# Kernel optimization log

Measured on AMD Instinct MI355X. Metric: run time of the kernel, lower is better.

The kernel has to match this reference:

```python
import jax, jax.numpy as jnp
import numpy as np
from functools import partial

TOP_K = 2
LN_EPS = 1e-5


def setup_inputs() -> dict:
    key = jax.random.key(0)
    ks = jax.random.split(key, 4)
    B, T, H, F, E = 2, 2048, 1024, 4096, 8
    hidden_states = jax.random.normal(ks[0], (B, T, H), dtype=jnp.float32)
    # Router weights: original inits to zeros; use small random so routing is non-degenerate.
    router_w = jax.random.normal(ks[1], (E, H), dtype=jnp.float32) * 0.02
    router_b = jnp.zeros((E,), dtype=jnp.float32)
    W1 = jax.random.normal(ks[2], (E, H, F), dtype=jnp.float32) * (1.0 / np.sqrt(H))
    b1 = jnp.zeros((E, F), dtype=jnp.float32)
    W2 = jax.random.normal(ks[3], (E, F, H), dtype=jnp.float32) * (1.0 / np.sqrt(F))
    b2 = jnp.zeros((E, H), dtype=jnp.float32)
    ln_gamma = jnp.ones((H,), dtype=jnp.float32)
    ln_beta = jnp.zeros((H,), dtype=jnp.float32)
    return {"hidden_states": hidden_states, "router_w": router_w, "router_b": router_b,
            "W1": W1, "b1": b1, "W2": W2, "b2": b2,
            "ln_gamma": ln_gamma, "ln_beta": ln_beta}


def _layer_norm(x, gamma, beta):
    mu = jnp.mean(x, axis=-1, keepdims=True)
    var = jnp.var(x, axis=-1, keepdims=True)
    return (x - mu) * jax.lax.rsqrt(var + LN_EPS) * gamma + beta


def _moe_forward(hidden_states, router_w, router_b, W1, b1, W2, b2, ln_gamma, ln_beta):
    B, T, H = hidden_states.shape
    E = router_w.shape[0]
    N = B * T
    x = hidden_states.reshape(N, H)
    # Router (jitter=0.0, eval mode): logits [N, E]
    logits = x @ router_w.T + router_b
    topk_vals, topk_idx = jax.lax.top_k(logits, TOP_K)        # [N, K]
    topk_w = jax.nn.softmax(topk_vals, axis=-1)               # [N, K]
    # Scatter top-k weights into a dense combine matrix [N, E] (zeros elsewhere).
    probs = jnp.zeros((N, E), dtype=x.dtype).at[jnp.arange(N)[:, None], topk_idx].set(topk_w)
    # Per-expert FFN via scan over the (small, fixed) expert axis; each step is one
    # big GEMM over all tokens weighted by that expert's combine prob (0 for
    # tokens not routed to it) — same math as gather/MLP/scatter with no capacity drop.
    def body(acc, params_e):
        Wa, ba, Wb, bb, pe = params_e          # pe: [N]
        h = jax.nn.gelu(x @ Wa + ba, approximate=False)   # [N, F]
        y = h @ Wb + bb                                    # [N, H]
        return acc + y * pe[:, None], None
    out, _ = jax.lax.scan(body, jnp.zeros_like(x), (W1, b1, W2, b2, probs.T))
    out = out.reshape(B, T, H)
    return _layer_norm(out + hidden_states, ln_gamma, ln_beta)


def reference(hidden_states, router_w, router_b, W1, b1, W2, b2, ln_gamma, ln_beta):
    return _moe_forward(hidden_states, router_w, router_b, W1, b1, W2, b2, ln_gamma, ln_beta)
```

## Files before the change

### kernel.cpp

```cpp
#include <hip/hip_runtime.h>
#include <hip/hip_bf16.h>


typedef unsigned short u16;
typedef unsigned int u32;
typedef __attribute__((ext_vector_type(4))) float f32x4;
typedef __attribute__((ext_vector_type(8))) short s16x8;
typedef __attribute__((ext_vector_type(8))) unsigned short u16x8;

#define GLD16(gp, lp) __builtin_amdgcn_global_load_lds( \
    (const __attribute__((address_space(1))) void*)(gp), \
    (__attribute__((address_space(3))) void*)(lp), 16, 0, 0)

__device__ __forceinline__ u16 f2bf(float f) {
    union { float f; u32 u; } v; v.f = f;
    u32 u = v.u;
    return (u16)((u + 0x7fffu + ((u >> 16) & 1u)) >> 16);
}

__device__ __forceinline__ float gelu_f(float v) {
    const float u = v * (0.7978845608f + 0.0356774081f * v * v);
    const float t = __expf(-2.0f * u);
    return v * __builtin_amdgcn_rcpf(1.0f + t);
}

__global__ void k_init(int* cc) { if (threadIdx.x < 16) cc[threadIdx.x] = 0; }

__global__ __launch_bounds__(256) void k_router(
    const float* __restrict__ x, const float* __restrict__ rw, const float* __restrict__ rb,
    u16* __restrict__ xb, int* __restrict__ eidx, float* __restrict__ wgt, int* __restrict__ counts)
{
    const int wav = threadIdx.x >> 6, lane = threadIdx.x & 63;
    const int t = blockIdx.x * 4 + wav;
    const float* xt = x + (size_t)t * 1024;
    float acc[8] = {0.f,0.f,0.f,0.f,0.f,0.f,0.f,0.f};
    #pragma unroll
    for (int c = 0; c < 4; c++) {
        const int base = c * 256 + lane * 4;
        const float4 xv = *(const float4*)(xt + base);
        ushort4 pk;
        pk.x = f2bf(xv.x); pk.y = f2bf(xv.y); pk.z = f2bf(xv.z); pk.w = f2bf(xv.w);
        *(ushort4*)(xb + (size_t)t * 1024 + base) = pk;
        #pragma unroll
        for (int e = 0; e < 8; e++) {
            const float4 wv = *(const float4*)(rw + e * 1024 + base);
            acc[e] += xv.x * wv.x + xv.y * wv.y + xv.z * wv.z + xv.w * wv.w;
        }
    }
    #pragma unroll
    for (int e = 0; e < 8; e++) {
        #pragma unroll
        for (int s = 32; s; s >>= 1) acc[e] += __shfl_xor(acc[e], s);
    }
    if (lane == 0) {
        float v0 = -3e38f, v1 = -3e38f; int i0 = 0, i1 = 0;
        #pragma unroll
        for (int e = 0; e < 8; e++) {
            const float l = acc[e] + rb[e];
            if (l > v0) { v1 = v0; i1 = i0; v0 = l; i0 = e; }
            else if (l > v1) { v1 = l; i1 = e; }
        }
        const float w0 = 1.0f / (1.0f + expf(v1 - v0));
        eidx[2 * t] = i0; eidx[2 * t + 1] = i1;
        wgt[2 * t] = w0; wgt[2 * t + 1] = 1.0f - w0;
        atomicAdd(&counts[i0], 1); atomicAdd(&counts[i1], 1);
    }
}

__global__ void k_offsets(const int* __restrict__ counts, int* __restrict__ offsets) {
    if (threadIdx.x == 0) {
        int s = 0;
        for (int e = 0; e < 8; e++) { offsets[e] = s; s += counts[e]; }
        offsets[8] = s;
    }
}

__global__ __launch_bounds__(256) void k_place(
    const int* __restrict__ eidx, const int* __restrict__ offsets, int* __restrict__ cursors,
    int* __restrict__ rows, int* __restrict__ pos_of)
{
    const int a = blockIdx.x * 256 + threadIdx.x;
    const int e = eidx[a];
    const int pos = offsets[e] + atomicAdd(&cursors[e], 1);
    rows[pos] = a >> 1;
    pos_of[a] = pos;
}

__global__ __launch_bounds__(256) void k_transp(
    const float* __restrict__ src, u16* __restrict__ dst, int R, int C)
{
    const int e = blockIdx.z;
    const float* s = src + (size_t)e * R * C;
    u16* d = dst + (size_t)e * R * C;
    const int c = blockIdx.x * 64 + (threadIdx.x >> 2);
    const int r0 = blockIdx.y * 32 + (threadIdx.x & 3) * 8;
    u16x8 v;
    #pragma unroll
    for (int k = 0; k < 8; k++)
        v[k] = f2bf(s[(size_t)(r0 + k) * C + c]);
    *(u16x8*)(d + (size_t)c * R + r0) = v;
}

__global__ __launch_bounds__(256) void k_gemm1(
    const u16* __restrict__ xb, const u16* __restrict__ W1t, const float* __restrict__ b1,
    u16* __restrict__ hbuf, const int* __restrict__ rows, const int* __restrict__ offsets)
{
    const int e = blockIdx.z;
    const int off = offsets[e], cnt = offsets[e + 1] - off;
    const int row0 = blockIdx.y * 128;
    if (row0 >= cnt) return;
    const int n0 = blockIdx.x * 128;
    const int tid = threadIdx.x;
    const int lane = tid & 63, wav = tid >> 6;

    __shared__ u16 At[128][32];
    __shared__ u16 Bt[128][32];

    const int ar0 = tid >> 2, ar1 = ar0 + 64;
    const int cl8 = (tid & 3) * 8;
    const int t0 = rows[off + min(row0 + ar0, cnt - 1)];
    const int t1 = rows[off + min(row0 + ar1, cnt - 1)];
    const u16* a_src0 = xb + (size_t)t0 * 1024 + cl8;
    const u16* a_src1 = xb + (size_t)t1 * 1024 + cl8;
    const u16* b_src0 = W1t + ((size_t)e * 4096 + n0 + ar0) * 1024 + cl8;
    const u16* b_src1 = W1t + ((size_t)e * 4096 + n0 + ar1) * 1024 + cl8;

    char* a_d0 = (char*)At + wav * 1024;
    char* a_d1 = (char*)At + 4096 + wav * 1024;
    char* b_d0 = (char*)Bt + wav * 1024;
    char* b_d1 = (char*)Bt + 4096 + wav * 1024;

    f32x4 acc[4][4] = {};
    const int wr = wav >> 1, wc = wav & 1;
    const int koff = (lane >> 4) * 8;
    const u16* Ab = &At[wr * 64 + (lane & 15)][koff];
    const u16* Bb = &Bt[wc * 64 + (lane & 15)][koff];

    for (int k0 = 0; k0 < 1024; k0 += 32) {
        GLD16(a_src0 + k0, a_d0);
        GLD16(a_src1 + k0, a_d1);
        GLD16(b_src0 + k0, b_d0);
        GLD16(b_src1 + k0, b_d1);
        __syncthreads();
        s16x8 af[4], bfr[4];
        #pragma unroll
        for (int i = 0; i < 4; i++) {
            af[i]  = *(const s16x8*)(Ab + i * 512);
            bfr[i] = *(const s16x8*)(Bb + i * 512);
        }
        #pragma unroll
        for (int mi = 0; mi < 4; mi++)
            #pragma unroll
            for (int ni = 0; ni < 4; ni++)
                acc[mi][ni] = __builtin_amdgcn_mfma_f32_16x16x32_bf16(af[mi], bfr[ni], acc[mi][ni], 0, 0, 0);
        __syncthreads();
    }

    const int rb4 = (lane >> 4) * 4;
    #pragma unroll
    for (int mi = 0; mi < 4; mi++) {
        #pragma unroll
        for (int j = 0; j < 4; j++) {
            const int lrow = wr * 64 + mi * 16 + rb4 + j;
            if (row0 + lrow < cnt) {
                const size_t gr = (size_t)(off + row0 + lrow);
                #pragma unroll
                for (int ni = 0; ni < 4; ni++) {
                    const int col = n0 + wc * 64 + ni * 16 + (lane & 15);
                    const float v = acc[mi][ni][j] + b1[e * 4096 + col];
                    hbuf[gr * 4096 + col] = f2bf(gelu_f(v));
                }
            }
        }
    }
}

__global__ __launch_bounds__(256) void k_gemm2(
    const u16* __restrict__ hbuf, const u16* __restrict__ W2t, const float* __restrict__ b2,
    float* __restrict__ y0, float* __restrict__ y1, const int* __restrict__ offsets)
{
    const int e = blockIdx.z >> 1, kh = blockIdx.z & 1;
    const int off = offsets[e], cnt = offsets[e + 1] - off;
    const int row0 = blockIdx.y * 128;
    if (row0 >= cnt) return;
    const int n0 = blockIdx.x * 128;
    const int tid = threadIdx.x;
    const int lane = tid & 63, wav = tid >> 6;
    const int kbase = kh * 2048;

    __shared__ u16 At[128][32];
    __shared__ u16 Bt[128][32];

    const int ar0 = tid >> 2, ar1 = ar0 + 64;
    const int cl8 = (tid & 3) * 8;
    const u16* a_src0 = hbuf + (size_t)(off + min(row0 + ar0, cnt - 1)) * 4096 + kbase + cl8;
    const u16* a_src1 = hbuf + (size_t)(off + min(row0 + ar1, cnt - 1)) * 4096 + kbase + cl8;
    const u16* b_src0 = W2t + ((size_t)e * 1024 + n0 + ar0) * 4096 + kbase + cl8;
    const u16* b_src1 = W2t + ((size_t)e * 1024 + n0 + ar1) * 4096 + kbase + cl8;

    char* a_d0 = (char*)At + wav * 1024;
    char* a_d1 = (char*)At + 4096 + wav * 1024;
    char* b_d0 = (char*)Bt + wav * 1024;
    char* b_d1 = (char*)Bt + 4096 + wav * 1024;

    f32x4 acc[4][4] = {};
    const int wr = wav >> 1, wc = wav & 1;
    const int koff = (lane >> 4) * 8;
    const u16* Ab = &At[wr * 64 + (lane & 15)][koff];
    const u16* Bb = &Bt[wc * 64 + (lane & 15)][koff];

    for (int k0 = 0; k0 < 2048; k0 += 32) {
        GLD16(a_src0 + k0, a_d0);
        GLD16(a_src1 + k0, a_d1);
        GLD16(b_src0 + k0, b_d0);
        GLD16(b_src1 + k0, b_d1);
        __syncthreads();
        s16x8 af[4], bfr[4];
        #pragma unroll
        for (int i = 0; i < 4; i++) {
            af[i]  = *(const s16x8*)(Ab + i * 512);
            bfr[i] = *(const s16x8*)(Bb + i * 512);
        }
        #pragma unroll
        for (int mi = 0; mi < 4; mi++)
            #pragma unroll
            for (int ni = 0; ni < 4; ni++)
                acc[mi][ni] = __builtin_amdgcn_mfma_f32_16x16x32_bf16(af[mi], bfr[ni], acc[mi][ni], 0, 0, 0);
        __syncthreads();
    }

    float* y = kh ? y1 : y0;
    const int rb4 = (lane >> 4) * 4;
    #pragma unroll
    for (int mi = 0; mi < 4; mi++) {
        #pragma unroll
        for (int j = 0; j < 4; j++) {
            const int lrow = wr * 64 + mi * 16 + rb4 + j;
            if (row0 + lrow < cnt) {
                const size_t gr = (size_t)(off + row0 + lrow);
                #pragma unroll
                for (int ni = 0; ni < 4; ni++) {
                    const int col = n0 + wc * 64 + ni * 16 + (lane & 15);
                    const float bias = kh ? 0.f : b2[e * 1024 + col];
                    y[gr * 1024 + col] = acc[mi][ni][j] + bias;
                }
            }
        }
    }
}

__global__ __launch_bounds__(256) void k_combine(
    const float* __restrict__ x, const float* __restrict__ y0, const float* __restrict__ y1,
    const int* __restrict__ pos_of, const float* __restrict__ wgt,
    const float* __restrict__ gamma, const float* __restrict__ beta,
    float* __restrict__ out)
{
    const int t = blockIdx.x;
    const int tid = threadIdx.x;
    const int p0 = pos_of[2 * t], p1 = pos_of[2 * t + 1];
    const float w0 = wgt[2 * t], w1 = wgt[2 * t + 1];
    const int j4 = tid * 4;
    const float4 xv = *(const float4*)(x + (size_t)t * 1024 + j4);
    const float4 ya0 = *(const float4*)(y0 + (size_t)p0 * 1024 + j4);
    const float4 yb0 = *(const float4*)(y1 + (size_t)p0 * 1024 + j4);
    const float4 ya1 = *(const float4*)(y0 + (size_t)p1 * 1024 + j4);
    const float4 yb1 = *(const float4*)(y1 + (size_t)p1 * 1024 + j4);
    float a0 = xv.x + w0 * (ya0.x + yb0.x) + w1 * (ya1.x + yb1.x);
    float a1 = xv.y + w0 * (ya0.y + yb0.y) + w1 * (ya1.y + yb1.y);
    float a2 = xv.z + w0 * (ya0.z + yb0.z) + w1 * (ya1.z + yb1.z);
    float a3 = xv.w + w0 * (ya0.w + yb0.w) + w1 * (ya1.w + yb1.w);
    float s = a0 + a1 + a2 + a3;
    float q = a0 * a0 + a1 * a1 + a2 * a2 + a3 * a3;
    #pragma unroll
    for (int o = 32; o; o >>= 1) { s += __shfl_xor(s, o); q += __shfl_xor(q, o); }
    __shared__ float ls[4], lq[4];
    const int wav = tid >> 6, lane = tid & 63;
    if (lane == 0) { ls[wav] = s; lq[wav] = q; }
    __syncthreads();
    s = ls[0] + ls[1] + ls[2] + ls[3];
    q = lq[0] + lq[1] + lq[2] + lq[3];
    const float mu = s * (1.0f / 1024.0f);
    const float var = q * (1.0f / 1024.0f) - mu * mu;
    const float rs = rsqrtf(var + 1e-5f);
    const float4 g = *(const float4*)(gamma + j4);
    const float4 b = *(const float4*)(beta + j4);
    float4 o4;
    o4.x = (a0 - mu) * rs * g.x + b.x;
    o4.y = (a1 - mu) * rs * g.y + b.y;
    o4.z = (a2 - mu) * rs * g.z + b.z;
    o4.w = (a3 - mu) * rs * g.w + b.w;
    *(float4*)(out + (size_t)t * 1024 + j4) = o4;
}

extern "C" void kernel_launch(void* const* d_in, const int* in_sizes, int n_in,
                              void* d_out, int out_size, void* d_ws, size_t ws_size,
                              hipStream_t stream) {
    const float* x     = (const float*)d_in[0];
    const float* rw    = (const float*)d_in[1];
    const float* rb    = (const float*)d_in[2];
    const float* W1    = (const float*)d_in[3];
    const float* b1    = (const float*)d_in[4];
    const float* W2    = (const float*)d_in[5];
    const float* b2    = (const float*)d_in[6];
    const float* gamma = (const float*)d_in[7];
    const float* beta  = (const float*)d_in[8];
    float* out = (float*)d_out;

    char* p = (char*)d_ws;
    auto alloc = [&](size_t bytes) { char* r = p; p += (bytes + 255) & ~(size_t)255; return r; };
    int*   counts  = (int*)alloc(16 * sizeof(int));
    int*   cursors = counts + 8;
    int*   offsets = (int*)alloc(9 * sizeof(int));
    int*   eidx    = (int*)alloc(8192 * sizeof(int));
    float* wgt     = (float*)alloc(8192 * sizeof(float));
    int*   pos_of  = (int*)alloc(8192 * sizeof(int));
    int*   rows    = (int*)alloc(8192 * sizeof(int));
    u16*   xb      = (u16*)alloc((size_t)4096 * 1024 * 2);
    u16*   W1t     = (u16*)alloc((size_t)8 * 4096 * 1024 * 2);
    u16*   W2t     = (u16*)alloc((size_t)8 * 1024 * 4096 * 2);
    u16*   hbuf    = (u16*)alloc((size_t)8192 * 4096 * 2);
    float* y0 = (float*)W1t;
    float* y1 = y0 + (size_t)8192 * 1024;

    hipLaunchKernelGGL(k_init, dim3(1), dim3(64), 0, stream, counts);
    hipLaunchKernelGGL(k_router, dim3(1024), dim3(256), 0, stream, x, rw, rb, xb, eidx, wgt, counts);
    hipLaunchKernelGGL(k_offsets, dim3(1), dim3(64), 0, stream, counts, offsets);
    hipLaunchKernelGGL(k_place, dim3(32), dim3(256), 0, stream, eidx, offsets, cursors, rows, pos_of);
    hipLaunchKernelGGL(k_transp, dim3(64, 32, 8), dim3(256), 0, stream, W1, W1t, 1024, 4096);
    hipLaunchKernelGGL(k_transp, dim3(16, 128, 8), dim3(256), 0, stream, W2, W2t, 4096, 1024);
    hipLaunchKernelGGL(k_gemm1, dim3(32, 32, 8), dim3(256), 0, stream, xb, W1t, b1, hbuf, rows, offsets);
    hipLaunchKernelGGL(k_gemm2, dim3(8, 32, 16), dim3(256), 0, stream, hbuf, W2t, b2, y0, y1, offsets);
    hipLaunchKernelGGL(k_combine, dim3(4096), dim3(256), 0, stream, x, y0, y1, pos_of, wgt, gamma, beta, out);
}
```

Baseline: 473.1 us.

## Double-buffer LDS in expert GEMMs, swizzle block order, hoist bias loads

Both expert GEMM kernels now keep two LDS buffers and issue the next K-tile's global-to-LDS loads before computing the current tile, with one barrier per iteration instead of two. The 3D grid is flattened to 1D and remapped so consecutive blocks go to different XCDs while blocks sharing an expert and weight tile stay grouped, aiming for better L2 reuse. Launch bounds now request 4 blocks per CU, and bias values are loaded once per thread before the epilogue. The cost is double the LDS per block and extra register pressure, which may limit occupancy.

```diff
diff --git a/kernel.cpp b/kernel.cpp
--- a/kernel.cpp
+++ b/kernel.cpp
@@ -101,20 +101,23 @@
     *(u16x8*)(d + (size_t)c * R + r0) = v;
 }
 
-__global__ __launch_bounds__(256) void k_gemm1(
+__global__ __launch_bounds__(256, 4) void k_gemm1(
     const u16* __restrict__ xb, const u16* __restrict__ W1t, const float* __restrict__ b1,
     u16* __restrict__ hbuf, const int* __restrict__ rows, const int* __restrict__ offsets)
 {
-    const int e = blockIdx.z;
+    const int fid = blockIdx.x;
+    const int swz = (fid & 7) * 1024 + (fid >> 3);
+    const int y = swz & 31, xx = (swz >> 5) & 31, e = swz >> 10;
+
     const int off = offsets[e], cnt = offsets[e + 1] - off;
-    const int row0 = blockIdx.y * 128;
+    const int row0 = y * 128;
     if (row0 >= cnt) return;
-    const int n0 = blockIdx.x * 128;
+    const int n0 = xx * 128;
     const int tid = threadIdx.x;
     const int lane = tid & 63, wav = tid >> 6;
 
-    __shared__ u16 At[128][32];
-    __shared__ u16 Bt[128][32];
+    __shared__ u16 At[2][128][32];
+    __shared__ u16 Bt[2][128][32];
 
     const int ar0 = tid >> 2, ar1 = ar0 + 64;
     const int cl8 = (tid & 3) * 8;
@@ -125,38 +128,51 @@
     const u16* b_src0 = W1t + ((size_t)e * 4096 + n0 + ar0) * 1024 + cl8;
     const u16* b_src1 = W1t + ((size_t)e * 4096 + n0 + ar1) * 1024 + cl8;
 
-    char* a_d0 = (char*)At + wav * 1024;
-    char* a_d1 = (char*)At + 4096 + wav * 1024;
-    char* b_d0 = (char*)Bt + wav * 1024;
-    char* b_d1 = (char*)Bt + 4096 + wav * 1024;
-
     f32x4 acc[4][4] = {};
     const int wr = wav >> 1, wc = wav & 1;
     const int koff = (lane >> 4) * 8;
-    const u16* Ab = &At[wr * 64 + (lane & 15)][koff];
-    const u16* Bb = &Bt[wc * 64 + (lane & 15)][koff];
-
-    for (int k0 = 0; k0 < 1024; k0 += 32) {
-        GLD16(a_src0 + k0, a_d0);
-        GLD16(a_src1 + k0, a_d1);
-        GLD16(b_src0 + k0, b_d0);
-        GLD16(b_src1 + k0, b_d1);
+    const u16* Ab = &At[0][wr * 64 + (lane & 15)][koff];
+    const u16* Bb = &Bt[0][wc * 64 + (lane & 15)][koff];
+
+    #define STAGE1(b, k0) { \
+        char* ad = (char*)At + (b) * 8192 + wav * 1024; \
+        char* bd = (char*)Bt + (b) * 8192 + wav * 1024; \
+        GLD16(a_src0 + (k0), ad); \
+        GLD16(a_src1 + (k0), ad + 4096); \
+        GLD16(b_src0 + (k0), bd); \
+        GLD16(b_src1 + (k0), bd + 4096); }
+
+    #define COMPUTE1(b) { \
+        const u16* Abp = Ab + (b) * 4096; \
+        const u16* Bbp = Bb + (b) * 4096; \
+        s16x8 af[4], bfr[4]; \
+        _Pragma("unroll") \
+        for (int i = 0; i < 4; i++) { \
+            af[i]  = *(const s16x8*)(Abp + i * 512); \
+            bfr[i] = *(const s16x8*)(Bbp + i * 512); \
+        } \
+        _Pragma("unroll") \
+        for (int mi = 0; mi < 4; mi++) \
+            _Pragma("unroll") \
+            for (int ni = 0; ni < 4; ni++) \
+                acc[mi][ni] = __builtin_amdgcn_mfma_f32_16x16x32_bf16(af[mi], bfr[ni], acc[mi][ni], 0, 0, 0); }
+
+    int b = 0;
+    STAGE1(0, 0);
+    __syncthreads();
+    for (int k0 = 32; k0 < 1024; k0 += 32) {
+        STAGE1(b ^ 1, k0);
+        COMPUTE1(b);
         __syncthreads();
-        s16x8 af[4], bfr[4];
-        #pragma unroll
-        for (int i = 0; i < 4; i++) {
-            af[i]  = *(const s16x8*)(Ab + i * 512);
-            bfr[i] = *(const s16x8*)(Bb + i * 512);
-        }
-        #pragma unroll
-        for (int mi = 0; mi < 4; mi++)
-            #pragma unroll
-            for (int ni = 0; ni < 4; ni++)
-                acc[mi][ni] = __builtin_amdgcn_mfma_f32_16x16x32_bf16(af[mi], bfr[ni], acc[mi][ni], 0, 0, 0);
-        __syncthreads();
-    }
+        b ^= 1;
+    }
+    COMPUTE1(b);
 
     const int rb4 = (lane >> 4) * 4;
+    const int colbase = n0 + wc * 64 + (lane & 15);
+    float bias[4];
+    #pragma unroll
+    for (int ni = 0; ni < 4; ni++) bias[ni] = b1[e * 4096 + colbase + ni * 16];
     #pragma unroll
     for (int mi = 0; mi < 4; mi++) {
         #pragma unroll
@@ -166,30 +182,33 @@
                 const size_t gr = (size_t)(off + row0 + lrow);
                 #pragma unroll
                 for (int ni = 0; ni < 4; ni++) {
-                    const int col = n0 + wc * 64 + ni * 16 + (lane & 15);
-                    const float v = acc[mi][ni][j] + b1[e * 4096 + col];
-                    hbuf[gr * 4096 + col] = f2bf(gelu_f(v));
+                    const float v = acc[mi][ni][j] + bias[ni];
+                    hbuf[gr * 4096 + colbase + ni * 16] = f2bf(gelu_f(v));
                 }
             }
         }
     }
 }
 
-__global__ __launch_bounds__(256) void k_gemm2(
+__global__ __launch_bounds__(256, 4) void k_gemm2(
     const u16* __restrict__ hbuf, const u16* __restrict__ W2t, const float* __restrict__ b2,
     float* __restrict__ y0, float* __restrict__ y1, const int* __restrict__ offsets)
 {
-    const int e = blockIdx.z >> 1, kh = blockIdx.z & 1;
+    const int fid = blockIdx.x;
+    const int swz = (fid & 7) * 512 + (fid >> 3);
+    const int y = swz & 31, xx = (swz >> 5) & 7, z = swz >> 8;
+    const int e = z >> 1, kh = z & 1;
+
     const int off = offsets[e], cnt = offsets[e + 1] - off;
-    const int row0 = blockIdx.y * 128;
+    const int row0 = y * 128;
     if (row0 >= cnt) return;
-    const int n0 = blockIdx.x * 128;
+    const int n0 = xx * 128;
     const int tid = threadIdx.x;
     const int lane = tid & 63, wav = tid >> 6;
     const int kbase = kh * 2048;
 
-    __shared__ u16 At[128][32];
-    __shared__ u16 Bt[128][32];
+    __shared__ u16 At[2][128][32];
+    __shared__ u16 Bt[2][128][32];
 
     const int ar0 = tid >> 2, ar1 = ar0 + 64;
     const int cl8 = (tid & 3) * 8;
@@ -198,39 +217,29 @@
     const u16* b_src0 = W2t + ((size_t)e * 1024 + n0 + ar0) * 4096 + kbase + cl8;
     const u16* b_src1 = W2t + ((size_t)e * 1024 + n0 + ar1) * 4096 + kbase + cl8;
 
-    char* a_d0 = (char*)At + wav * 1024;
-    char* a_d1 = (char*)At + 4096 + wav * 1024;
-    char* b_d0 = (char*)Bt + wav * 1024;
-    char* b_d1 = (char*)Bt + 4096 + wav * 1024;
-
     f32x4 acc[4][4] = {};
     const int wr = wav >> 1, wc = wav & 1;
     const int koff = (lane >> 4) * 8;
-    const u16* Ab = &At[wr * 64 + (lane & 15)][koff];
-    const u16* Bb = &Bt[wc * 64 + (lane & 15)][koff];
-
-    for (int k0 = 0; k0 < 2048; k0 += 32) {
-        GLD16(a_src0 + k0, a_d0);
-        GLD16(a_src1 + k0, a_d1);
-        GLD16(b_src0 + k0, b_d0);
-        GLD16(b_src1 + k0, b_d1);
+    const u16* Ab = &At[0][wr * 64 + (lane & 15)][koff];
+    const u16* Bb = &Bt[0][wc * 64 + (lane & 15)][koff];
+
+    int b = 0;
+    STAGE1(0, 0);
+    __syncthreads();
+    for (int k0 = 32; k0 < 2048; k0 += 32) {
+        STAGE1(b ^ 1, k0);
+        COMPUTE1(b);
         __syncthreads();
-        s16x8 af[4], bfr[4];
-        #pragma unroll
-        for (int i = 0; i < 4; i++) {
-            af[i]  = *(const s16x8*)(Ab + i * 512);
-            bfr[i] = *(const s16x8*)(Bb + i * 512);
-        }
-        #pragma unroll
-        for (int mi = 0; mi < 4; mi++)
-            #pragma unroll
-            for (int ni = 0; ni < 4; ni++)
-                acc[mi][ni] = __builtin_amdgcn_mfma_f32_16x16x32_bf16(af[mi], bfr[ni], acc[mi][ni], 0, 0, 0);
-        __syncthreads();
-    }
-
-    float* y = kh ? y1 : y0;
+        b ^= 1;
+    }
+    COMPUTE1(b);
+
+    float* yy = kh ? y1 : y0;
     const int rb4 = (lane >> 4) * 4;
+    const int colbase = n0 + wc * 64 + (lane & 15);
+    float bias[4];
+    #pragma unroll
+    for (int ni = 0; ni < 4; ni++) bias[ni] = kh ? 0.f : b2[e * 1024 + colbase + ni * 16];
     #pragma unroll
     for (int mi = 0; mi < 4; mi++) {
         #pragma unroll
@@ -239,11 +248,8 @@
             if (row0 + lrow < cnt) {
                 const size_t gr = (size_t)(off + row0 + lrow);
                 #pragma unroll
-                for (int ni = 0; ni < 4; ni++) {
-                    const int col = n0 + wc * 64 + ni * 16 + (lane & 15);
-                    const float bias = kh ? 0.f : b2[e * 1024 + col];
-                    y[gr * 1024 + col] = acc[mi][ni][j] + bias;
-                }
+                for (int ni = 0; ni < 4; ni++)
+                    yy[gr * 1024 + colbase + ni * 16] = acc[mi][ni][j] + bias[ni];
             }
         }
     }
@@ -328,7 +334,7 @@
     hipLaunchKernelGGL(k_place, dim3(32), dim3(256), 0, stream, eidx, offsets, cursors, rows, pos_of);
     hipLaunchKernelGGL(k_transp, dim3(64, 32, 8), dim3(256), 0, stream, W1, W1t, 1024, 4096);
     hipLaunchKernelGGL(k_transp, dim3(16, 128, 8), dim3(256), 0, stream, W2, W2t, 4096, 1024);
-    hipLaunchKernelGGL(k_gemm1, dim3(32, 32, 8), dim3(256), 0, stream, xb, W1t, b1, hbuf, rows, offsets);
-    hipLaunchKernelGGL(k_gemm2, dim3(8, 32, 16), dim3(256), 0, stream, hbuf, W2t, b2, y0, y1, offsets);
+    hipLaunchKernelGGL(k_gemm1, dim3(8192), dim3(256), 0, stream, xb, W1t, b1, hbuf, rows, offsets);
+    hipLaunchKernelGGL(k_gemm2, dim3(4096), dim3(256), 0, stream, hbuf, W2t, b2, y0, y1, offsets);
     hipLaunchKernelGGL(k_combine, dim3(4096), dim3(256), 0, stream, x, y0, y1, pos_of, wgt, gamma, beta, out);
 }
```

New measurement: 477.6 us. Within noise of the previous version (+1.0%).
